# Optimization experiments

Hardware: AMD Instinct MI355X
Metric: run time of the kernel (lower is better)

## Reference

```python
import jax, jax.numpy as jnp
import numpy as np

N = 100000   # nodes
E = 1600000  # directed edges (before self-loops)
D_IN, D_HID, D_OUT = 128, 128, 16


def _glorot(key, shape):
    lim = np.sqrt(6.0 / (shape[0] + shape[1])).astype(np.float32)
    return jax.random.uniform(key, shape, jnp.float32, -lim, lim)


def setup_inputs() -> dict:
    key = jax.random.key(0)
    ks = jax.random.split(key, 5)
    x = jax.random.normal(ks[0], (N, D_IN), jnp.float32)
    edge_index = jax.random.randint(ks[1], (2, E), 0, N, dtype=jnp.int32)
    return {
        "x": x,
        "edge_index": edge_index,
        "W1": _glorot(ks[2], (D_IN, D_HID)),
        "b1": jnp.zeros((D_HID,), jnp.float32),
        "W2": _glorot(ks[3], (D_HID, D_HID)),
        "b2": jnp.zeros((D_HID,), jnp.float32),
        "W3": _glorot(ks[4], (D_HID, D_OUT)),
        "b3": jnp.zeros((D_OUT,), jnp.float32),
    }


def _gcn_conv(x, W, b, src, dst, norm):
    # GCNConv: linear transform, then normalized sum-aggregation into dst, then bias.
    h = x @ W                                    # [N, Dout]
    msg = h[src] * norm[:, None]                 # [E+N, Dout] gathered messages
    return jax.ops.segment_sum(msg, dst, num_segments=N) + b


def reference(x, edge_index, W1, b1, W2, b2, W3, b3):
    # add self-loops (PyG GCNConv default add_self_loops=True)
    loops = jnp.arange(N, dtype=edge_index.dtype)
    src = jnp.concatenate([edge_index[0], loops])
    dst = jnp.concatenate([edge_index[1], loops])
    # symmetric normalization D^{-1/2} (A+I) D^{-1/2}; degree over destinations
    deg = jax.ops.segment_sum(jnp.ones_like(dst, jnp.float32), dst, num_segments=N)
    dis = jnp.where(deg > 0, jax.lax.rsqrt(jnp.maximum(deg, 1.0)), 0.0)
    norm = dis[src] * dis[dst]

    h = jax.nn.relu(_gcn_conv(x, W1, b1, src, dst, norm))   # dropout is identity in eval mode
    h = jax.nn.relu(_gcn_conv(h, W2, b2, src, dst, norm))
    return _gcn_conv(h, W3, b3, src, dst, norm)
```

## Files before the change

kernel.cpp:

```cpp
#include <hip/hip_runtime.h>

#define NN 100000
#define EE 1600000
#define DH 128
#define DO 16
#define NBLK1 98

__global__ __launch_bounds__(256) void k_zero(int* __restrict__ meta) {
    int v = blockIdx.x * 256 + threadIdx.x;
    if (v < NN) meta[v] = 0;
}

__global__ __launch_bounds__(256) void k_hist(const int* __restrict__ dst,
                                              int* __restrict__ meta) {
    int e = blockIdx.x * 256 + threadIdx.x;
    if (e < EE) atomicAdd(meta + dst[e], 1);
}

__global__ __launch_bounds__(1024) void k_scan1(int* __restrict__ meta,
                                                int* __restrict__ bsum) {
    __shared__ int sm[1024];
    const int t = threadIdx.x;
    const int idx = blockIdx.x * 1024 + t;
    int c = (idx < NN) ? meta[idx] : 0;
    int v = c;
    sm[t] = v;
    __syncthreads();
    for (int off = 1; off < 1024; off <<= 1) {
        int add = (t >= off) ? sm[t - off] : 0;
        __syncthreads();
        v += add;
        sm[t] = v;
        __syncthreads();
    }
    if (t == 1023) bsum[blockIdx.x] = v;
    if (idx < NN) meta[idx] = v - c;
}

__global__ __launch_bounds__(128) void k_scan2(int* __restrict__ bsum) {
    __shared__ int sm[128];
    const int t = threadIdx.x;
    int c = (t < NBLK1) ? bsum[t] : 0;
    int v = c;
    sm[t] = v;
    __syncthreads();
    for (int off = 1; off < 128; off <<= 1) {
        int add = (t >= off) ? sm[t - off] : 0;
        __syncthreads();
        v += add;
        sm[t] = v;
        __syncthreads();
    }
    if (t < NBLK1) bsum[t] = v - c;
}

__global__ __launch_bounds__(256) void k_scan3(int* __restrict__ meta,
                                               const int* __restrict__ bsum) {
    int idx = blockIdx.x * 256 + threadIdx.x;
    if (idx < NN) meta[idx] += bsum[idx >> 10];
}

__global__ __launch_bounds__(256) void k_scatter(const int* __restrict__ ei,
                                                 int* __restrict__ meta,
                                                 int* __restrict__ cs) {
    int e = blockIdx.x * 256 + threadIdx.x;
    if (e < EE) {
        int d = ei[EE + e];
        int pos = atomicAdd(meta + d, 1);
        cs[pos] = ei[e];
    }
}

__device__ __forceinline__ float4 relu4(float4 a) {
    a.x = fmaxf(a.x, 0.f); a.y = fmaxf(a.y, 0.f);
    a.z = fmaxf(a.z, 0.f); a.w = fmaxf(a.w, 0.f);
    return a;
}

template <bool RELU>
__global__ __launch_bounds__(256) void k_gemm128(const float* __restrict__ in,
                                                 const float* __restrict__ W,
                                                 const int* __restrict__ meta,
                                                 float* __restrict__ out) {
    __shared__ float Wl[DH * DH];
    for (int i = threadIdx.x * 4; i < DH * DH; i += 256 * 4)
        *(float4*)(Wl + i) = *(const float4*)(W + i);
    __syncthreads();

    const int wid  = threadIdx.x >> 6;
    const int lane = threadIdx.x & 63;
    const int gw   = blockIdx.x * 4 + wid;
    const int strd = gridDim.x * 4;

    for (int rb = gw * 4; rb < NN; rb += strd * 4) {
        const int rbu = __builtin_amdgcn_readfirstlane(rb);
        const float* x0 = in + (size_t)rbu * DH;
        float2 acc0 = {0.f, 0.f}, acc1 = {0.f, 0.f};
        float2 acc2 = {0.f, 0.f}, acc3 = {0.f, 0.f};

        for (int k = 0; k < DH; k += 4) {
            float4 a0 = *(const float4*)(x0 + 0 * DH + k);
            float4 a1 = *(const float4*)(x0 + 1 * DH + k);
            float4 a2 = *(const float4*)(x0 + 2 * DH + k);
            float4 a3 = *(const float4*)(x0 + 3 * DH + k);
            if (RELU) { a0 = relu4(a0); a1 = relu4(a1); a2 = relu4(a2); a3 = relu4(a3); }

            float2 w0 = *(const float2*)(Wl + (k + 0) * DH + lane * 2);
            float2 w1 = *(const float2*)(Wl + (k + 1) * DH + lane * 2);
            float2 w2 = *(const float2*)(Wl + (k + 2) * DH + lane * 2);
            float2 w3 = *(const float2*)(Wl + (k + 3) * DH + lane * 2);

            acc0.x = fmaf(a0.x, w0.x, acc0.x); acc0.y = fmaf(a0.x, w0.y, acc0.y);
            acc0.x = fmaf(a0.y, w1.x, acc0.x); acc0.y = fmaf(a0.y, w1.y, acc0.y);
            acc0.x = fmaf(a0.z, w2.x, acc0.x); acc0.y = fmaf(a0.z, w2.y, acc0.y);
            acc0.x = fmaf(a0.w, w3.x, acc0.x); acc0.y = fmaf(a0.w, w3.y, acc0.y);

            acc1.x = fmaf(a1.x, w0.x, acc1.x); acc1.y = fmaf(a1.x, w0.y, acc1.y);
            acc1.x = fmaf(a1.y, w1.x, acc1.x); acc1.y = fmaf(a1.y, w1.y, acc1.y);
            acc1.x = fmaf(a1.z, w2.x, acc1.x); acc1.y = fmaf(a1.z, w2.y, acc1.y);
            acc1.x = fmaf(a1.w, w3.x, acc1.x); acc1.y = fmaf(a1.w, w3.y, acc1.y);

            acc2.x = fmaf(a2.x, w0.x, acc2.x); acc2.y = fmaf(a2.x, w0.y, acc2.y);
            acc2.x = fmaf(a2.y, w1.x, acc2.x); acc2.y = fmaf(a2.y, w1.y, acc2.y);
            acc2.x = fmaf(a2.z, w2.x, acc2.x); acc2.y = fmaf(a2.z, w2.y, acc2.y);
            acc2.x = fmaf(a2.w, w3.x, acc2.x); acc2.y = fmaf(a2.w, w3.y, acc2.y);

            acc3.x = fmaf(a3.x, w0.x, acc3.x); acc3.y = fmaf(a3.x, w0.y, acc3.y);
            acc3.x = fmaf(a3.y, w1.x, acc3.x); acc3.y = fmaf(a3.y, w1.y, acc3.y);
            acc3.x = fmaf(a3.z, w2.x, acc3.x); acc3.y = fmaf(a3.z, w2.y, acc3.y);
            acc3.x = fmaf(a3.w, w3.x, acc3.x); acc3.y = fmaf(a3.w, w3.y, acc3.y);
        }

        const int b0 = (rbu == 0) ? 0 : meta[rbu - 1];
        const int e0 = meta[rbu + 0];
        const int e1 = meta[rbu + 1];
        const int e2 = meta[rbu + 2];
        const int e3 = meta[rbu + 3];
        const float d0 = 1.0f / sqrtf((float)(e0 - b0 + 1));
        const float d1 = 1.0f / sqrtf((float)(e1 - e0 + 1));
        const float d2 = 1.0f / sqrtf((float)(e2 - e1 + 1));
        const float d3 = 1.0f / sqrtf((float)(e3 - e2 + 1));
        acc0.x *= d0; acc0.y *= d0;
        acc1.x *= d1; acc1.y *= d1;
        acc2.x *= d2; acc2.y *= d2;
        acc3.x *= d3; acc3.y *= d3;

        *(float2*)(out + (size_t)(rbu + 0) * DH + lane * 2) = acc0;
        *(float2*)(out + (size_t)(rbu + 1) * DH + lane * 2) = acc1;
        *(float2*)(out + (size_t)(rbu + 2) * DH + lane * 2) = acc2;
        *(float2*)(out + (size_t)(rbu + 3) * DH + lane * 2) = acc3;
    }
}

template <bool RELU>
__global__ __launch_bounds__(256) void k_gemm16(const float* __restrict__ in,
                                                const float* __restrict__ W,
                                                const int* __restrict__ meta,
                                                float* __restrict__ out) {
    __shared__ float Wl[DH * DO];
    for (int i = threadIdx.x * 4; i < DH * DO; i += 256 * 4)
        *(float4*)(Wl + i) = *(const float4*)(W + i);
    __syncthreads();

    const int lane = threadIdx.x & 63;
    const int col  = lane & 15;
    const int rsub = lane >> 4;
    const int gw   = blockIdx.x * 4 + (threadIdx.x >> 6);
    const int strd = gridDim.x * 4;

    for (int rb = gw * 4; rb < NN; rb += strd * 4) {
        int row = rb + rsub;
        const float* x0 = in + (size_t)row * DH;
        float acc = 0.f;
        for (int k = 0; k < DH; k += 4) {
            float4 a = *(const float4*)(x0 + k);
            if (RELU) a = relu4(a);
            acc = fmaf(a.x, Wl[(k + 0) * DO + col], acc);
            acc = fmaf(a.y, Wl[(k + 1) * DO + col], acc);
            acc = fmaf(a.z, Wl[(k + 2) * DO + col], acc);
            acc = fmaf(a.w, Wl[(k + 3) * DO + col], acc);
        }
        const int e  = meta[row];
        const int bg = (row == 0) ? 0 : meta[row - 1];
        const float dl = 1.0f / sqrtf((float)(e - bg + 1));
        out[(size_t)row * DO + col] = acc * dl;
    }
}

__global__ __launch_bounds__(256) void k_agg128(const float* __restrict__ msg,
                                                const int* __restrict__ meta,
                                                const int* __restrict__ cs,
                                                const float* __restrict__ b,
                                                float* __restrict__ out) {
    const int wid  = threadIdx.x >> 6;
    const int lane = threadIdx.x & 63;
    const float2 bb = *(const float2*)(b + lane * 2);
    const int d = blockIdx.x * 4 + wid;
    if (d >= NN) return;
    const int du  = __builtin_amdgcn_readfirstlane(d);
    const int end = meta[du];
    const int beg = (du == 0) ? 0 : meta[du - 1];
    const float dd = 1.0f / sqrtf((float)(end - beg + 1));

    float2 acc = *((const float2*)(msg + (size_t)du * DH) + lane);

    int j = beg;
    for (; j + 4 <= end; j += 4) {
        int s0 = cs[j], s1 = cs[j + 1], s2 = cs[j + 2], s3 = cs[j + 3];
        float2 v0 = *((const float2*)(msg + (size_t)s0 * DH) + lane);
        float2 v1 = *((const float2*)(msg + (size_t)s1 * DH) + lane);
        float2 v2 = *((const float2*)(msg + (size_t)s2 * DH) + lane);
        float2 v3 = *((const float2*)(msg + (size_t)s3 * DH) + lane);
        acc.x += (v0.x + v1.x) + (v2.x + v3.x);
        acc.y += (v0.y + v1.y) + (v2.y + v3.y);
    }
    for (; j < end; ++j) {
        int s0 = cs[j];
        float2 v0 = *((const float2*)(msg + (size_t)s0 * DH) + lane);
        acc.x += v0.x; acc.y += v0.y;
    }
    float2 o; o.x = bb.x + dd * acc.x; o.y = bb.y + dd * acc.y;
    *((float2*)(out + (size_t)du * DH) + lane) = o;
}

__global__ __launch_bounds__(256) void k_agg16(const float* __restrict__ msg,
                                               const int* __restrict__ meta,
                                               const int* __restrict__ cs,
                                               const float* __restrict__ b,
                                               float* __restrict__ out) {
    int i = blockIdx.x * 256 + threadIdx.x;
    if (i >= NN * DO) return;
    const int v   = i >> 4;
    const int col = i & 15;
    const int end = meta[v];
    const int beg = (v == 0) ? 0 : meta[v - 1];
    const float dd = 1.0f / sqrtf((float)(end - beg + 1));

    float acc = msg[(size_t)v * DO + col];
    int j = beg;
    for (; j + 4 <= end; j += 4) {
        int s0 = cs[j], s1 = cs[j + 1], s2 = cs[j + 2], s3 = cs[j + 3];
        acc += (msg[(size_t)s0 * DO + col] + msg[(size_t)s1 * DO + col])
             + (msg[(size_t)s2 * DO + col] + msg[(size_t)s3 * DO + col]);
    }
    for (; j < end; ++j) acc += msg[(size_t)cs[j] * DO + col];
    out[i] = b[col] + dd * acc;
}

extern "C" void kernel_launch(void* const* d_in, const int* in_sizes, int n_in,
                              void* d_out, int out_size, void* d_ws, size_t ws_size,
                              hipStream_t stream) {
    (void)in_sizes; (void)n_in; (void)out_size; (void)ws_size;
    const float* x  = (const float*)d_in[0];
    const int*   ei = (const int*)d_in[1];
    const float* W1 = (const float*)d_in[2];
    const float* b1 = (const float*)d_in[3];
    const float* W2 = (const float*)d_in[4];
    const float* b2 = (const float*)d_in[5];
    const float* W3 = (const float*)d_in[6];
    const float* b3 = (const float*)d_in[7];
    float* out = (float*)d_out;

    int*   meta = (int*)d_ws;
    int*   baux = meta + NN;
    int*   cs   = baux + 128;
    float* A    = (float*)(cs + EE);
    float* B    = A + (size_t)NN * DH;
    float* C    = A;

    k_zero   <<<391, 256, 0, stream>>>(meta);
    k_hist   <<<6250, 256, 0, stream>>>(ei + EE, meta);
    k_scan1  <<<NBLK1, 1024, 0, stream>>>(meta, baux);
    k_scan2  <<<1, 128, 0, stream>>>(baux);
    k_scan3  <<<391, 256, 0, stream>>>(meta, baux);
    k_scatter<<<6250, 256, 0, stream>>>(ei, meta, cs);

    k_gemm128<false><<<6250, 256, 0, stream>>>(x, W1, meta, A);
    k_agg128<<<25000, 256, 0, stream>>>(A, meta, cs, b1, B);

    k_gemm128<true><<<6250, 256, 0, stream>>>(B, W2, meta, A);
    k_agg128<<<25000, 256, 0, stream>>>(A, meta, cs, b2, B);

    k_gemm16<true><<<6250, 256, 0, stream>>>(B, W3, meta, C);
    k_agg16<<<6250, 256, 0, stream>>>(C, meta, cs, b3, out);
}
```

Measured before the change: 915.9 us.

## Retile 128-wide GEMM to 16 rows per wave and fuse ReLU into aggregation

The 128x128 GEMM now gives each wavefront 16 consecutive rows instead of 4. Each weight pair read from LDS is reused across 16 rows, and the kernel runs as a persistent grid of 512 blocks with 512 threads that each copy W into LDS once. ReLU moves from the GEMM input into the aggregation kernel's output, so the next layer reads activations that are already rectified. The wider accumulator array (32 floats plus loads) raises register pressure and may lower occupancy. The 16 rows per wave are loaded as strided float2 reads, which may coalesce poorly.

After: 962.3 us. 1.05x slower.

```diff
diff --git a/kernel.cpp b/kernel.cpp
--- a/kernel.cpp
+++ b/kernel.cpp
@@ -71,88 +71,52 @@
     }
 }
 
-__device__ __forceinline__ float4 relu4(float4 a) {
-    a.x = fmaxf(a.x, 0.f); a.y = fmaxf(a.y, 0.f);
-    a.z = fmaxf(a.z, 0.f); a.w = fmaxf(a.w, 0.f);
-    return a;
-}
-
-template <bool RELU>
-__global__ __launch_bounds__(256) void k_gemm128(const float* __restrict__ in,
+__global__ __launch_bounds__(512) void k_gemm128(const float* __restrict__ in,
                                                  const float* __restrict__ W,
                                                  const int* __restrict__ meta,
                                                  float* __restrict__ out) {
     __shared__ float Wl[DH * DH];
-    for (int i = threadIdx.x * 4; i < DH * DH; i += 256 * 4)
+    for (int i = threadIdx.x * 4; i < DH * DH; i += 512 * 4)
         *(float4*)(Wl + i) = *(const float4*)(W + i);
     __syncthreads();
 
     const int wid  = threadIdx.x >> 6;
     const int lane = threadIdx.x & 63;
-    const int gw   = blockIdx.x * 4 + wid;
-    const int strd = gridDim.x * 4;
-
-    for (int rb = gw * 4; rb < NN; rb += strd * 4) {
+    const int c2   = lane * 2;
+
+    for (int rb = blockIdx.x * 128 + wid * 16; rb < NN; rb += gridDim.x * 128) {
         const int rbu = __builtin_amdgcn_readfirstlane(rb);
         const float* x0 = in + (size_t)rbu * DH;
-        float2 acc0 = {0.f, 0.f}, acc1 = {0.f, 0.f};
-        float2 acc2 = {0.f, 0.f}, acc3 = {0.f, 0.f};
-
-        for (int k = 0; k < DH; k += 4) {
-            float4 a0 = *(const float4*)(x0 + 0 * DH + k);
-            float4 a1 = *(const float4*)(x0 + 1 * DH + k);
-            float4 a2 = *(const float4*)(x0 + 2 * DH + k);
-            float4 a3 = *(const float4*)(x0 + 3 * DH + k);
-            if (RELU) { a0 = relu4(a0); a1 = relu4(a1); a2 = relu4(a2); a3 = relu4(a3); }
-
-            float2 w0 = *(const float2*)(Wl + (k + 0) * DH + lane * 2);
-            float2 w1 = *(const float2*)(Wl + (k + 1) * DH + lane * 2);
-            float2 w2 = *(const float2*)(Wl + (k + 2) * DH + lane * 2);
-            float2 w3 = *(const float2*)(Wl + (k + 3) * DH + lane * 2);
-
-            acc0.x = fmaf(a0.x, w0.x, acc0.x); acc0.y = fmaf(a0.x, w0.y, acc0.y);
-            acc0.x = fmaf(a0.y, w1.x, acc0.x); acc0.y = fmaf(a0.y, w1.y, acc0.y);
-            acc0.x = fmaf(a0.z, w2.x, acc0.x); acc0.y = fmaf(a0.z, w2.y, acc0.y);
-            acc0.x = fmaf(a0.w, w3.x, acc0.x); acc0.y = fmaf(a0.w, w3.y, acc0.y);
-
-            acc1.x = fmaf(a1.x, w0.x, acc1.x); acc1.y = fmaf(a1.x, w0.y, acc1.y);
-            acc1.x = fmaf(a1.y, w1.x, acc1.x); acc1.y = fmaf(a1.y, w1.y, acc1.y);
-            acc1.x = fmaf(a1.z, w2.x, acc1.x); acc1.y = fmaf(a1.z, w2.y, acc1.y);
-            acc1.x = fmaf(a1.w, w3.x, acc1.x); acc1.y = fmaf(a1.w, w3.y, acc1.y);
-
-            acc2.x = fmaf(a2.x, w0.x, acc2.x); acc2.y = fmaf(a2.x, w0.y, acc2.y);
-            acc2.x = fmaf(a2.y, w1.x, acc2.x); acc2.y = fmaf(a2.y, w1.y, acc2.y);
-            acc2.x = fmaf(a2.z, w2.x, acc2.x); acc2.y = fmaf(a2.z, w2.y, acc2.y);
-            acc2.x = fmaf(a2.w, w3.x, acc2.x); acc2.y = fmaf(a2.w, w3.y, acc2.y);
-
-            acc3.x = fmaf(a3.x, w0.x, acc3.x); acc3.y = fmaf(a3.x, w0.y, acc3.y);
-            acc3.x = fmaf(a3.y, w1.x, acc3.x); acc3.y = fmaf(a3.y, w1.y, acc3.y);
-            acc3.x = fmaf(a3.z, w2.x, acc3.x); acc3.y = fmaf(a3.z, w2.y, acc3.y);
-            acc3.x = fmaf(a3.w, w3.x, acc3.x); acc3.y = fmaf(a3.w, w3.y, acc3.y);
+
+        float2 acc[16];
+        #pragma unroll
+        for (int i = 0; i < 16; ++i) { acc[i].x = 0.f; acc[i].y = 0.f; }
+
+        for (int k = 0; k < DH; k += 2) {
+            const float2 w0 = *(const float2*)(Wl + (k + 0) * DH + c2);
+            const float2 w1 = *(const float2*)(Wl + (k + 1) * DH + c2);
+            #pragma unroll
+            for (int i = 0; i < 16; ++i) {
+                const float2 a = *(const float2*)(x0 + i * DH + k);
+                acc[i].x = fmaf(a.x, w0.x, acc[i].x);
+                acc[i].y = fmaf(a.x, w0.y, acc[i].y);
+                acc[i].x = fmaf(a.y, w1.x, acc[i].x);
+                acc[i].y = fmaf(a.y, w1.y, acc[i].y);
+            }
         }
 
         const int b0 = (rbu == 0) ? 0 : meta[rbu - 1];
-        const int e0 = meta[rbu + 0];
-        const int e1 = meta[rbu + 1];
-        const int e2 = meta[rbu + 2];
-        const int e3 = meta[rbu + 3];
-        const float d0 = 1.0f / sqrtf((float)(e0 - b0 + 1));
-        const float d1 = 1.0f / sqrtf((float)(e1 - e0 + 1));
-        const float d2 = 1.0f / sqrtf((float)(e2 - e1 + 1));
-        const float d3 = 1.0f / sqrtf((float)(e3 - e2 + 1));
-        acc0.x *= d0; acc0.y *= d0;
-        acc1.x *= d1; acc1.y *= d1;
-        acc2.x *= d2; acc2.y *= d2;
-        acc3.x *= d3; acc3.y *= d3;
-
-        *(float2*)(out + (size_t)(rbu + 0) * DH + lane * 2) = acc0;
-        *(float2*)(out + (size_t)(rbu + 1) * DH + lane * 2) = acc1;
-        *(float2*)(out + (size_t)(rbu + 2) * DH + lane * 2) = acc2;
-        *(float2*)(out + (size_t)(rbu + 3) * DH + lane * 2) = acc3;
-    }
-}
-
-template <bool RELU>
+        #pragma unroll
+        for (int i = 0; i < 16; ++i) {
+            const int e_i = meta[rbu + i];
+            const int bg  = (i == 0) ? b0 : meta[rbu + i - 1];
+            const float dl = 1.0f / sqrtf((float)(e_i - bg + 1));
+            acc[i].x *= dl; acc[i].y *= dl;
+            *(float2*)(out + (size_t)(rbu + i) * DH + c2) = acc[i];
+        }
+    }
+}
+
 __global__ __launch_bounds__(256) void k_gemm16(const float* __restrict__ in,
                                                 const float* __restrict__ W,
                                                 const int* __restrict__ meta,
@@ -174,7 +138,6 @@
         float acc = 0.f;
         for (int k = 0; k < DH; k += 4) {
             float4 a = *(const float4*)(x0 + k);
-            if (RELU) a = relu4(a);
             acc = fmaf(a.x, Wl[(k + 0) * DO + col], acc);
             acc = fmaf(a.y, Wl[(k + 1) * DO + col], acc);
             acc = fmaf(a.z, Wl[(k + 2) * DO + col], acc);
@@ -187,6 +150,7 @@
     }
 }
 
+template <bool RELU_OUT>
 __global__ __launch_bounds__(256) void k_agg128(const float* __restrict__ msg,
                                                 const int* __restrict__ meta,
                                                 const int* __restrict__ cs,
@@ -220,6 +184,7 @@
         acc.x += v0.x; acc.y += v0.y;
     }
     float2 o; o.x = bb.x + dd * acc.x; o.y = bb.y + dd * acc.y;
+    if (RELU_OUT) { o.x = fmaxf(o.x, 0.f); o.y = fmaxf(o.y, 0.f); }
     *((float2*)(out + (size_t)du * DH) + lane) = o;
 }
 
@@ -275,12 +240,12 @@
     k_scan3  <<<391, 256, 0, stream>>>(meta, baux);
     k_scatter<<<6250, 256, 0, stream>>>(ei, meta, cs);
 
-    k_gemm128<false><<<6250, 256, 0, stream>>>(x, W1, meta, A);
-    k_agg128<<<25000, 256, 0, stream>>>(A, meta, cs, b1, B);
-
-    k_gemm128<true><<<6250, 256, 0, stream>>>(B, W2, meta, A);
-    k_agg128<<<25000, 256, 0, stream>>>(A, meta, cs, b2, B);
-
-    k_gemm16<true><<<6250, 256, 0, stream>>>(B, W3, meta, C);
+    k_gemm128<<<512, 512, 0, stream>>>(x, W1, meta, A);
+    k_agg128<true><<<25000, 256, 0, stream>>>(A, meta, cs, b1, B);
+
+    k_gemm128<<<512, 512, 0, stream>>>(B, W2, meta, A);
+    k_agg128<true><<<25000, 256, 0, stream>>>(A, meta, cs, b2, B);
+
+    k_gemm16<<<6250, 256, 0, stream>>>(B, W3, meta, C);
     k_agg16<<<6250, 256, 0, stream>>>(C, meta, cs, b3, out);
 }
```

## Split GEMM128 columns across block pairs and fuse ReLU into aggregation

Applied to the files above, without the earlier changes.

The 128-wide GEMM now loads only a 64-column half of W into shared memory (32 KB instead of 64 KB). Each block pair covers both halves of a 64-row tile, and the 512-thread blocks use a launch bound of 4 blocks per SM to raise occupancy. ReLU moves from the GEMM input loads into the aggregation epilogue, so each activation gets it once rather than once per consumer. The trade-off is that each input row is now read twice, once per column-half block.

Measured after the change: 821.7 us. -10.3%, faster.

```diff
diff --git a/kernel.cpp b/kernel.cpp
--- a/kernel.cpp
+++ b/kernel.cpp
@@ -71,88 +71,87 @@
     }
 }
 
-__device__ __forceinline__ float4 relu4(float4 a) {
-    a.x = fmaxf(a.x, 0.f); a.y = fmaxf(a.y, 0.f);
-    a.z = fmaxf(a.z, 0.f); a.w = fmaxf(a.w, 0.f);
-    return a;
-}
-
-template <bool RELU>
-__global__ __launch_bounds__(256) void k_gemm128(const float* __restrict__ in,
-                                                 const float* __restrict__ W,
-                                                 const int* __restrict__ meta,
-                                                 float* __restrict__ out) {
-    __shared__ float Wl[DH * DH];
-    for (int i = threadIdx.x * 4; i < DH * DH; i += 256 * 4)
-        *(float4*)(Wl + i) = *(const float4*)(W + i);
+__global__ __launch_bounds__(512, 4) void k_gemm128(const float* __restrict__ in,
+                                                    const float* __restrict__ W,
+                                                    const int* __restrict__ meta,
+                                                    float* __restrict__ out) {
+    __shared__ float Wl[DH * 64];
+    const int colbase = (blockIdx.x & 1) * 64;
+    for (int i = threadIdx.x * 4; i < DH * 64; i += 512 * 4) {
+        const int r = i >> 6;
+        const int c = i & 63;
+        *(float4*)(Wl + i) = *(const float4*)(W + r * DH + colbase + c);
+    }
     __syncthreads();
 
     const int wid  = threadIdx.x >> 6;
     const int lane = threadIdx.x & 63;
-    const int gw   = blockIdx.x * 4 + wid;
-    const int strd = gridDim.x * 4;
-
-    for (int rb = gw * 4; rb < NN; rb += strd * 4) {
-        const int rbu = __builtin_amdgcn_readfirstlane(rb);
-        const float* x0 = in + (size_t)rbu * DH;
-        float2 acc0 = {0.f, 0.f}, acc1 = {0.f, 0.f};
-        float2 acc2 = {0.f, 0.f}, acc3 = {0.f, 0.f};
-
-        for (int k = 0; k < DH; k += 4) {
-            float4 a0 = *(const float4*)(x0 + 0 * DH + k);
-            float4 a1 = *(const float4*)(x0 + 1 * DH + k);
-            float4 a2 = *(const float4*)(x0 + 2 * DH + k);
-            float4 a3 = *(const float4*)(x0 + 3 * DH + k);
-            if (RELU) { a0 = relu4(a0); a1 = relu4(a1); a2 = relu4(a2); a3 = relu4(a3); }
-
-            float2 w0 = *(const float2*)(Wl + (k + 0) * DH + lane * 2);
-            float2 w1 = *(const float2*)(Wl + (k + 1) * DH + lane * 2);
-            float2 w2 = *(const float2*)(Wl + (k + 2) * DH + lane * 2);
-            float2 w3 = *(const float2*)(Wl + (k + 3) * DH + lane * 2);
-
-            acc0.x = fmaf(a0.x, w0.x, acc0.x); acc0.y = fmaf(a0.x, w0.y, acc0.y);
-            acc0.x = fmaf(a0.y, w1.x, acc0.x); acc0.y = fmaf(a0.y, w1.y, acc0.y);
-            acc0.x = fmaf(a0.z, w2.x, acc0.x); acc0.y = fmaf(a0.z, w2.y, acc0.y);
-            acc0.x = fmaf(a0.w, w3.x, acc0.x); acc0.y = fmaf(a0.w, w3.y, acc0.y);
-
-            acc1.x = fmaf(a1.x, w0.x, acc1.x); acc1.y = fmaf(a1.x, w0.y, acc1.y);
-            acc1.x = fmaf(a1.y, w1.x, acc1.x); acc1.y = fmaf(a1.y, w1.y, acc1.y);
-            acc1.x = fmaf(a1.z, w2.x, acc1.x); acc1.y = fmaf(a1.z, w2.y, acc1.y);
-            acc1.x = fmaf(a1.w, w3.x, acc1.x); acc1.y = fmaf(a1.w, w3.y, acc1.y);
-
-            acc2.x = fmaf(a2.x, w0.x, acc2.x); acc2.y = fmaf(a2.x, w0.y, acc2.y);
-            acc2.x = fmaf(a2.y, w1.x, acc2.x); acc2.y = fmaf(a2.y, w1.y, acc2.y);
-            acc2.x = fmaf(a2.z, w2.x, acc2.x); acc2.y = fmaf(a2.z, w2.y, acc2.y);
-            acc2.x = fmaf(a2.w, w3.x, acc2.x); acc2.y = fmaf(a2.w, w3.y, acc2.y);
-
-            acc3.x = fmaf(a3.x, w0.x, acc3.x); acc3.y = fmaf(a3.x, w0.y, acc3.y);
-            acc3.x = fmaf(a3.y, w1.x, acc3.x); acc3.y = fmaf(a3.y, w1.y, acc3.y);
-            acc3.x = fmaf(a3.z, w2.x, acc3.x); acc3.y = fmaf(a3.z, w2.y, acc3.y);
-            acc3.x = fmaf(a3.w, w3.x, acc3.x); acc3.y = fmaf(a3.w, w3.y, acc3.y);
-        }
-
-        const int b0 = (rbu == 0) ? 0 : meta[rbu - 1];
-        const int e0 = meta[rbu + 0];
-        const int e1 = meta[rbu + 1];
-        const int e2 = meta[rbu + 2];
-        const int e3 = meta[rbu + 3];
-        const float d0 = 1.0f / sqrtf((float)(e0 - b0 + 1));
-        const float d1 = 1.0f / sqrtf((float)(e1 - e0 + 1));
-        const float d2 = 1.0f / sqrtf((float)(e2 - e1 + 1));
-        const float d3 = 1.0f / sqrtf((float)(e3 - e2 + 1));
-        acc0.x *= d0; acc0.y *= d0;
-        acc1.x *= d1; acc1.y *= d1;
-        acc2.x *= d2; acc2.y *= d2;
-        acc3.x *= d3; acc3.y *= d3;
-
-        *(float2*)(out + (size_t)(rbu + 0) * DH + lane * 2) = acc0;
-        *(float2*)(out + (size_t)(rbu + 1) * DH + lane * 2) = acc1;
-        *(float2*)(out + (size_t)(rbu + 2) * DH + lane * 2) = acc2;
-        *(float2*)(out + (size_t)(rbu + 3) * DH + lane * 2) = acc3;
-    }
-}
-
-template <bool RELU>
+    const int cp   = lane & 31;
+    const int rh   = lane >> 5;
+    const int c2   = cp * 2;
+
+    const int rbw = (blockIdx.x >> 1) * 64 + wid * 8;
+    if (rbw >= NN) return;
+
+    const int r0 = rbw + rh * 4;
+    const float* x0 = in + (size_t)r0 * DH;
+
+    float2 acc0 = {0.f, 0.f}, acc1 = {0.f, 0.f};
+    float2 acc2 = {0.f, 0.f}, acc3 = {0.f, 0.f};
+
+    for (int k = 0; k < DH; k += 4) {
+        const float4 a0 = *(const float4*)(x0 + 0 * DH + k);
+        const float4 a1 = *(const float4*)(x0 + 1 * DH + k);
+        const float4 a2 = *(const float4*)(x0 + 2 * DH + k);
+        const float4 a3 = *(const float4*)(x0 + 3 * DH + k);
+
+        const float2 w0 = *(const float2*)(Wl + (k + 0) * 64 + c2);
+        const float2 w1 = *(const float2*)(Wl + (k + 1) * 64 + c2);
+        const float2 w2 = *(const float2*)(Wl + (k + 2) * 64 + c2);
+        const float2 w3 = *(const float2*)(Wl + (k + 3) * 64 + c2);
+
+        acc0.x = fmaf(a0.x, w0.x, acc0.x); acc0.y = fmaf(a0.x, w0.y, acc0.y);
+        acc0.x = fmaf(a0.y, w1.x, acc0.x); acc0.y = fmaf(a0.y, w1.y, acc0.y);
+        acc0.x = fmaf(a0.z, w2.x, acc0.x); acc0.y = fmaf(a0.z, w2.y, acc0.y);
+        acc0.x = fmaf(a0.w, w3.x, acc0.x); acc0.y = fmaf(a0.w, w3.y, acc0.y);
+
+        acc1.x = fmaf(a1.x, w0.x, acc1.x); acc1.y = fmaf(a1.x, w0.y, acc1.y);
+        acc1.x = fmaf(a1.y, w1.x, acc1.x); acc1.y = fmaf(a1.y, w1.y, acc1.y);
+        acc1.x = fmaf(a1.z, w2.x, acc1.x); acc1.y = fmaf(a1.z, w2.y, acc1.y);
+        acc1.x = fmaf(a1.w, w3.x, acc1.x); acc1.y = fmaf(a1.w, w3.y, acc1.y);
+
+        acc2.x = fmaf(a2.x, w0.x, acc2.x); acc2.y = fmaf(a2.x, w0.y, acc2.y);
+        acc2.x = fmaf(a2.y, w1.x, acc2.x); acc2.y = fmaf(a2.y, w1.y, acc2.y);
+        acc2.x = fmaf(a2.z, w2.x, acc2.x); acc2.y = fmaf(a2.z, w2.y, acc2.y);
+        acc2.x = fmaf(a2.w, w3.x, acc2.x); acc2.y = fmaf(a2.w, w3.y, acc2.y);
+
+        acc3.x = fmaf(a3.x, w0.x, acc3.x); acc3.y = fmaf(a3.x, w0.y, acc3.y);
+        acc3.x = fmaf(a3.y, w1.x, acc3.x); acc3.y = fmaf(a3.y, w1.y, acc3.y);
+        acc3.x = fmaf(a3.z, w2.x, acc3.x); acc3.y = fmaf(a3.z, w2.y, acc3.y);
+        acc3.x = fmaf(a3.w, w3.x, acc3.x); acc3.y = fmaf(a3.w, w3.y, acc3.y);
+    }
+
+    const int bprev = (r0 == 0) ? 0 : meta[r0 - 1];
+    const int e0 = meta[r0 + 0];
+    const int e1 = meta[r0 + 1];
+    const int e2 = meta[r0 + 2];
+    const int e3 = meta[r0 + 3];
+    const float d0 = 1.0f / sqrtf((float)(e0 - bprev + 1));
+    const float d1 = 1.0f / sqrtf((float)(e1 - e0 + 1));
+    const float d2 = 1.0f / sqrtf((float)(e2 - e1 + 1));
+    const float d3 = 1.0f / sqrtf((float)(e3 - e2 + 1));
+    acc0.x *= d0; acc0.y *= d0;
+    acc1.x *= d1; acc1.y *= d1;
+    acc2.x *= d2; acc2.y *= d2;
+    acc3.x *= d3; acc3.y *= d3;
+
+    float* o0 = out + (size_t)r0 * DH + colbase + c2;
+    *(float2*)(o0 + 0 * DH) = acc0;
+    *(float2*)(o0 + 1 * DH) = acc1;
+    *(float2*)(o0 + 2 * DH) = acc2;
+    *(float2*)(o0 + 3 * DH) = acc3;
+}
+
 __global__ __launch_bounds__(256) void k_gemm16(const float* __restrict__ in,
                                                 const float* __restrict__ W,
                                                 const int* __restrict__ meta,
@@ -174,7 +173,6 @@
         float acc = 0.f;
         for (int k = 0; k < DH; k += 4) {
             float4 a = *(const float4*)(x0 + k);
-            if (RELU) a = relu4(a);
             acc = fmaf(a.x, Wl[(k + 0) * DO + col], acc);
             acc = fmaf(a.y, Wl[(k + 1) * DO + col], acc);
             acc = fmaf(a.z, Wl[(k + 2) * DO + col], acc);
@@ -187,6 +185,7 @@
     }
 }
 
+template <bool RELU_OUT>
 __global__ __launch_bounds__(256) void k_agg128(const float* __restrict__ msg,
                                                 const int* __restrict__ meta,
                                                 const int* __restrict__ cs,
@@ -220,6 +219,7 @@
         acc.x += v0.x; acc.y += v0.y;
     }
     float2 o; o.x = bb.x + dd * acc.x; o.y = bb.y + dd * acc.y;
+    if (RELU_OUT) { o.x = fmaxf(o.x, 0.f); o.y = fmaxf(o.y, 0.f); }
     *((float2*)(out + (size_t)du * DH) + lane) = o;
 }
 
@@ -275,12 +275,14 @@
     k_scan3  <<<391, 256, 0, stream>>>(meta, baux);
     k_scatter<<<6250, 256, 0, stream>>>(ei, meta, cs);
 
-    k_gemm128<false><<<6250, 256, 0, stream>>>(x, W1, meta, A);
-    k_agg128<<<25000, 256, 0, stream>>>(A, meta, cs, b1, B);
-
-    k_gemm128<true><<<6250, 256, 0, stream>>>(B, W2, meta, A);
-    k_agg128<<<25000, 256, 0, stream>>>(A, meta, cs, b2, B);
-
-    k_gemm16<true><<<6250, 256, 0, stream>>>(B, W3, meta, C);
+    const int G128 = 1563 * 2;
+
+    k_gemm128<<<G128, 512, 0, stream>>>(x, W1, meta, A);
+    k_agg128<true><<<25000, 256, 0, stream>>>(A, meta, cs, b1, B);
+
+    k_gemm128<<<G128, 512, 0, stream>>>(B, W2, meta, A);
+    k_agg128<true><<<25000, 256, 0, stream>>>(A, meta, cs, b2, B);
+
+    k_gemm16<<<6250, 256, 0, stream>>>(B, W3, meta, C);
     k_agg16<<<6250, 256, 0, stream>>>(C, meta, cs, b3, out);
 }
```
